# Optimization experiments

Hardware: AMD Instinct MI355X
Metric: run time of the kernel (lower is better)

Reference implementation:

```python
import jax, jax.numpy as jnp
import numpy as np

VISION_TOKEN_TYPE = 1
B, L, D, FF = 2, 2048, 1024, 4096


def setup_inputs() -> dict:
    key = jax.random.key(0)
    ks = jax.random.split(key, 8)
    s_in = 1.0 / np.sqrt(D)
    s_ff = 1.0 / np.sqrt(FF)
    return {
        "hidden_states": jax.random.normal(ks[0], (B, L, D), dtype=jnp.float32),
        "token_type_ids": jax.random.randint(ks[1], (B, L), 0, 2, dtype=jnp.int64),
        "v_gate": jax.random.normal(ks[2], (FF, D), dtype=jnp.float32) * s_in,
        "v_up": jax.random.normal(ks[3], (FF, D), dtype=jnp.float32) * s_in,
        "v_down": jax.random.normal(ks[4], (D, FF), dtype=jnp.float32) * s_ff,
        "l_gate": jax.random.normal(ks[5], (FF, D), dtype=jnp.float32) * s_in,
        "l_up": jax.random.normal(ks[6], (FF, D), dtype=jnp.float32) * s_in,
        "l_down": jax.random.normal(ks[7], (D, FF), dtype=jnp.float32) * s_ff,
    }


def _swiglu_mlp(x, w_gate, w_up, w_down):
    # x: (B, L, D); torch Linear stores weight as (out, in) -> contract on last dim
    g = jax.nn.silu(jnp.einsum("bld,fd->blf", x, w_gate))
    u = jnp.einsum("bld,fd->blf", x, w_up)
    return jnp.einsum("blf,df->bld", g * u, w_down)


def _vision_mask(token_type_ids):
    # vision token iff this token AND the next token are vision type; last col False
    t = token_type_ids == VISION_TOKEN_TYPE
    inner = t[:, :-1] & t[:, 1:]
    return jnp.concatenate([inner, jnp.zeros((t.shape[0], 1), dtype=bool)], axis=1)


def reference(hidden_states, token_type_ids, v_gate, v_up, v_down, l_gate, l_up, l_down):
    vision_mask = _vision_mask(token_type_ids)  # (B, L) bool
    vis_out = _swiglu_mlp(hidden_states, v_gate, v_up, v_down)
    lang_out = _swiglu_mlp(hidden_states, l_gate, l_up, l_down)
    return jnp.where(vision_mask[:, :, None], vis_out, lang_out)
```

## Files before the change

### kernel.cpp

```cpp
#include <hip/hip_runtime.h>
#include <hip/hip_bf16.h>
#include <stdint.h>


#define TOKENS 4096
#define SEQ    2048
#define DIM    1024
#define FFDIM  4096
#define MAXPAD 4608

typedef __attribute__((ext_vector_type(8))) short bf16x8;
typedef __attribute__((ext_vector_type(4))) float f32x4;

#define GAS __attribute__((address_space(1)))
#define LAS __attribute__((address_space(3)))

__device__ inline unsigned short f2bf(float x) {
    union { float f; unsigned int u; } c; c.f = x;
    unsigned int r = c.u + 0x7FFFu + ((c.u >> 16) & 1u);
    return (unsigned short)(r >> 16);
}
__device__ inline float bf2f(unsigned short u) {
    union { unsigned int i; float f; } c; c.i = ((unsigned int)u) << 16;
    return c.f;
}

struct __align__(16) us8 { unsigned short v[8]; };

__global__ __launch_bounds__(1024) void scan_kernel(const int* __restrict__ tt,
                                                    int* __restrict__ src_of,
                                                    int* __restrict__ counts) {
    __shared__ int wsum[16];
    const int tid  = threadIdx.x;
    const int lane = tid & 63;
    const int wav  = tid >> 6;

    for (int i = tid; i < MAXPAD; i += 1024) src_of[i] = -1;

    const int t0 = tid * 4;
    int v[4], cnt = 0;
#pragma unroll
    for (int j = 0; j < 4; ++j) {
        const int t = t0 + j;
        const int l = t & (SEQ - 1);
        int vis = 0;
        if (l < SEQ - 1) vis = (tt[t] == 1) & (tt[t + 1] == 1);
        v[j] = vis; cnt += vis;
    }

    int s = cnt;
#pragma unroll
    for (int off = 1; off < 64; off <<= 1) {
        const int o = __shfl_up(s, off, 64);
        if (lane >= off) s += o;
    }
    if (lane == 63) wsum[wav] = s;
    __syncthreads();
    if (wav == 0 && lane < 16) {
        int w = wsum[lane];
#pragma unroll
        for (int off = 1; off < 16; off <<= 1) {
            const int o = __shfl_up(w, off, 16);
            if (lane >= off) w += o;
        }
        wsum[lane] = w;
    }
    __syncthreads();

    const int wbase  = wav ? wsum[wav - 1] : 0;
    const int incl   = wbase + s;
    const int excl   = incl - cnt;
    const int totalV = wsum[15];
    const int padNv  = (totalV + 127) & ~127;
    int pv = excl;
    int pl = padNv + (t0 - excl);
#pragma unroll
    for (int j = 0; j < 4; ++j) {
        const int t = t0 + j;
        if (v[j]) src_of[pv++] = t; else src_of[pl++] = t;
    }
    if (tid == 0) {
        const int Nl = TOKENS - totalV;
        counts[0] = padNv;
        counts[1] = padNv + ((Nl + 127) & ~127);
    }
}

__device__ inline void gather_body(const float* __restrict__ hs, const int* __restrict__ src_of,
                                   unsigned short* __restrict__ Xg, int gid) {
    const int row = gid >> 7;
    const int c   = (gid & 127) * 8;
    const int src = src_of[row];
    us8 o;
    if (src >= 0) {
        const float4 a = *reinterpret_cast<const float4*>(hs + (size_t)src * DIM + c);
        const float4 b = *reinterpret_cast<const float4*>(hs + (size_t)src * DIM + c + 4);
        o.v[0] = f2bf(a.x); o.v[1] = f2bf(a.y); o.v[2] = f2bf(a.z); o.v[3] = f2bf(a.w);
        o.v[4] = f2bf(b.x); o.v[5] = f2bf(b.y); o.v[6] = f2bf(b.z); o.v[7] = f2bf(b.w);
    } else {
#pragma unroll
        for (int j = 0; j < 8; ++j) o.v[j] = 0;
    }
    *reinterpret_cast<us8*>(Xg + (size_t)row * DIM + c) = o;
}

__global__ void gather_cast(const float* __restrict__ hs, const int* __restrict__ src_of,
                            unsigned short* __restrict__ Xg) {
    gather_body(hs, src_of, Xg, blockIdx.x * 256 + threadIdx.x);
}

__device__ inline void cast8(const float* __restrict__ in, unsigned short* __restrict__ out, int i) {
    const float4 a = *reinterpret_cast<const float4*>(in + i);
    const float4 b = *reinterpret_cast<const float4*>(in + i + 4);
    us8 o;
    o.v[0] = f2bf(a.x); o.v[1] = f2bf(a.y); o.v[2] = f2bf(a.z); o.v[3] = f2bf(a.w);
    o.v[4] = f2bf(b.x); o.v[5] = f2bf(b.y); o.v[6] = f2bf(b.z); o.v[7] = f2bf(b.w);
    *reinterpret_cast<us8*>(out + i) = o;
}

__global__ void prep_kernel(const float* __restrict__ hs, const int* __restrict__ src_of,
                            unsigned short* __restrict__ Xg,
                            const float* __restrict__ s0, const float* __restrict__ s1,
                            const float* __restrict__ s2, const float* __restrict__ s3,
                            const float* __restrict__ s4, const float* __restrict__ s5,
                            unsigned short* __restrict__ d0, unsigned short* __restrict__ d1,
                            unsigned short* __restrict__ d2, unsigned short* __restrict__ d3,
                            unsigned short* __restrict__ d4, unsigned short* __restrict__ d5) {
    const int m = blockIdx.y;
    if (m == 0) {
        gather_body(hs, src_of, Xg, blockIdx.x * 256 + threadIdx.x);
    } else {
        const int i = (blockIdx.x * 256 + threadIdx.x) * 8;
        if (i >= FFDIM * DIM) return;
        const float* s = (m == 1) ? s0 : (m == 2) ? s1 : (m == 3) ? s2 : (m == 4) ? s3 : (m == 5) ? s4 : s5;
        unsigned short* d = (m == 1) ? d0 : (m == 2) ? d1 : (m == 3) ? d2 : (m == 4) ? d3 : (m == 5) ? d4 : d5;
        cast8(s, d, i);
    }
}

__global__ void cast4_kernel(const float* __restrict__ s0, const float* __restrict__ s1,
                             const float* __restrict__ s2, const float* __restrict__ s3,
                             unsigned short* __restrict__ d0, unsigned short* __restrict__ d1,
                             unsigned short* __restrict__ d2, unsigned short* __restrict__ d3) {
    const int i = (blockIdx.x * 256 + threadIdx.x) * 8;
    const int m = blockIdx.y;
    const float* s = (m == 0) ? s0 : (m == 1) ? s1 : (m == 2) ? s2 : s3;
    unsigned short* d = (m == 0) ? d0 : (m == 1) ? d1 : (m == 2) ? d2 : d3;
    cast8(s, d, i);
}

__global__ void cast2_kernel(const float* __restrict__ s0, const float* __restrict__ s1,
                             unsigned short* __restrict__ d0, unsigned short* __restrict__ d1) {
    const int i = (blockIdx.x * 256 + threadIdx.x) * 8;
    const float* s = blockIdx.y ? s1 : s0;
    unsigned short* d = blockIdx.y ? d1 : d0;
    cast8(s, d, i);
}

__global__ __launch_bounds__(256, 2) void gemm_p1(
    const unsigned short* __restrict__ A,
    const unsigned short* __restrict__ B0_v, const unsigned short* __restrict__ B1_v,
    const unsigned short* __restrict__ B0_l, const unsigned short* __restrict__ B1_l,
    unsigned short* __restrict__ H,
    const int* __restrict__ counts)
{
    __shared__ unsigned short Ls[256 * 64];

    const int m0 = blockIdx.y * 128;
    const int padNv = counts[0], padTot = counts[1];
    if (m0 >= padTot) return;
    const int expert = (m0 >= padNv);
    const unsigned short* B0 = expert ? B0_l : B0_v;
    const unsigned short* B1 = expert ? B1_l : B1_v;

    const int tid  = threadIdx.x;
    const int wid  = tid >> 6;
    const int lane = tid & 63;
    const int n0   = blockIdx.x * 64;

    constexpr int NI = 8;
    const unsigned short* src[NI];
    int loff[NI];
    const int cs = ((lane & 7) ^ (lane >> 3)) * 8;
#pragma unroll
    for (int i = 0; i < NI; ++i) {
        const int g = wid * 64 + i * 8 + (lane >> 3);
        const unsigned short* p;
        if (g < 128) {
            p = A + (size_t)(m0 + g) * DIM;
        } else {
            const int br = g - 128;
            p = (br < 64) ? (B0 + (size_t)(n0 + br) * DIM) : (B1 + (size_t)(n0 + br - 64) * DIM);
        }
        src[i] = p + cs;
        loff[i] = (wid * 64 + i * 8) * 64;
    }

    const int rlo = lane & 15;
    const int sw7 = rlo & 7;

    f32x4 acc[2][8];
#pragma unroll
    for (int i = 0; i < 2; ++i)
#pragma unroll
        for (int j = 0; j < 8; ++j)
            acc[i][j] = (f32x4){0.f, 0.f, 0.f, 0.f};

    const int NKT = DIM / 64;
#pragma unroll 1
    for (int kt = 0; kt < NKT; ++kt) {
        if (kt) __syncthreads();
        const int c = kt * 64;
#pragma unroll
        for (int i = 0; i < NI; ++i)
            __builtin_amdgcn_global_load_lds((const GAS void*)(src[i] + c),
                                             (LAS void*)&Ls[loff[i]], 16, 0, 0);
        asm volatile("s_waitcnt vmcnt(0)" ::: "memory");
        __syncthreads();

#pragma unroll
        for (int kh = 0; kh < 2; ++kh) {
            const int kc    = (lane >> 4) + kh * 4;
            const int swoff = (kc ^ sw7) * 8;
            const bf16x8 af0 = *reinterpret_cast<const bf16x8*>(&Ls[(wid * 32 + rlo) * 64 + swoff]);
            const bf16x8 af1 = *reinterpret_cast<const bf16x8*>(&Ls[(wid * 32 + 16 + rlo) * 64 + swoff]);
#pragma unroll
            for (int n = 0; n < 8; ++n) {
                const bf16x8 bfr = *reinterpret_cast<const bf16x8*>(&Ls[(128 + n * 16 + rlo) * 64 + swoff]);
                acc[0][n] = __builtin_amdgcn_mfma_f32_16x16x32_bf16(af0, bfr, acc[0][n], 0, 0, 0);
                acc[1][n] = __builtin_amdgcn_mfma_f32_16x16x32_bf16(af1, bfr, acc[1][n], 0, 0, 0);
            }
        }
    }

    const int rbase = m0 + wid * 32 + ((lane >> 4) * 4);
    const int cin   = lane & 15;
#pragma unroll
    for (int fr = 0; fr < 2; ++fr)
#pragma unroll
        for (int reg = 0; reg < 4; ++reg) {
            const int row = rbase + fr * 16 + reg;
#pragma unroll
            for (int n = 0; n < 4; ++n) {
                const float g = acc[fr][n][reg];
                const float u = acc[fr][n + 4][reg];
                const float h = g / (1.0f + __expf(-g)) * u;
                H[(size_t)row * FFDIM + n0 + n * 16 + cin] = f2bf(h);
            }
        }
}

__global__ __launch_bounds__(256, 2) void gemm_p2(
    const unsigned short* __restrict__ A,
    const unsigned short* __restrict__ Bd_v, const unsigned short* __restrict__ Bd_l,
    unsigned short* __restrict__ P,
    const int* __restrict__ counts)
{
    __shared__ unsigned short Ls[2][256 * 64];

    const int m0 = blockIdx.y * 128;
    const int padNv = counts[0], padTot = counts[1];
    if (m0 >= padTot) return;
    const unsigned short* B0 = (m0 >= padNv) ? Bd_l : Bd_v;

    const int tid  = threadIdx.x;
    const int wid  = tid >> 6;
    const int lane = tid & 63;
    const int wr   = wid >> 1;
    const int wc   = wid & 1;
    const int n0   = blockIdx.x * 128;
    const int kbase = blockIdx.z * (FFDIM / 2);

    constexpr int NI = 8;
    const unsigned short* src[NI];
    int loff[NI];
    const int cs = ((lane & 7) ^ (lane >> 3)) * 8;
#pragma unroll
    for (int i = 0; i < NI; ++i) {
        const int g = wid * 64 + i * 8 + (lane >> 3);
        const unsigned short* p = (g < 128)
            ? A + (size_t)(m0 + g) * FFDIM
            : B0 + (size_t)(n0 + g - 128) * FFDIM;
        src[i] = p + kbase + cs;
        loff[i] = (wid * 64 + i * 8) * 64;
    }

#define STAGE2(buf, kkt) do { \
    const int _c = (kkt) * 64; \
    _Pragma("unroll") \
    for (int i = 0; i < NI; ++i) \
        __builtin_amdgcn_global_load_lds((const GAS void*)(src[i] + _c), \
                                         (LAS void*)&Ls[buf][loff[i]], 16, 0, 0); \
} while (0)

    const int rlo = lane & 15;
    const int sw7 = rlo & 7;

    f32x4 acc[4][4];
#pragma unroll
    for (int i = 0; i < 4; ++i)
#pragma unroll
        for (int j = 0; j < 4; ++j)
            acc[i][j] = (f32x4){0.f, 0.f, 0.f, 0.f};

    STAGE2(0, 0);

    const int NKT = (FFDIM / 2) / 64;
    bf16x8 af[4], bf[4];
#pragma unroll 1
    for (int kt = 0; kt < NKT; ++kt) {
        const int cur = kt & 1;

        asm volatile("" ::: "memory");
        __builtin_amdgcn_s_barrier();
        asm volatile("" ::: "memory");

        if (kt + 1 < NKT) {
            STAGE2(cur ^ 1, kt + 1);
            asm volatile("s_waitcnt vmcnt(8)" ::: "memory");
        } else {
            asm volatile("s_waitcnt vmcnt(0)" ::: "memory");
        }

        asm volatile("" ::: "memory");
        __builtin_amdgcn_s_barrier();
        asm volatile("" ::: "memory");

#pragma unroll
        for (int kh = 0; kh < 2; ++kh) {
            const int kc    = (lane >> 4) + kh * 4;
            const int swoff = (kc ^ sw7) * 8;
#pragma unroll
            for (int i = 0; i < 4; ++i)
                af[i] = *reinterpret_cast<const bf16x8*>(&Ls[cur][(wr * 64 + i * 16 + rlo) * 64 + swoff]);
#pragma unroll
            for (int j = 0; j < 4; ++j)
                bf[j] = *reinterpret_cast<const bf16x8*>(&Ls[cur][(128 + wc * 64 + j * 16 + rlo) * 64 + swoff]);

            __builtin_amdgcn_s_setprio(1);
#pragma unroll
            for (int i = 0; i < 4; ++i)
#pragma unroll
                for (int j = 0; j < 4; ++j)
                    acc[i][j] = __builtin_amdgcn_mfma_f32_16x16x32_bf16(af[i], bf[j], acc[i][j], 0, 0, 0);
            __builtin_amdgcn_s_setprio(0);
        }
    }
#undef STAGE2

    unsigned short* Pz = P + (size_t)blockIdx.z * MAXPAD * DIM;
    const int rbase = m0 + wr * 64 + ((lane >> 4) * 4);
    const int cin   = lane & 15;
#pragma unroll
    for (int i = 0; i < 4; ++i)
#pragma unroll
        for (int reg = 0; reg < 4; ++reg) {
            const int row = rbase + i * 16 + reg;
#pragma unroll
            for (int j = 0; j < 4; ++j)
                Pz[(size_t)row * DIM + n0 + wc * 64 + j * 16 + cin] = f2bf(acc[i][j][reg]);
        }
}

__global__ void reduce_kernel(const unsigned short* __restrict__ P,
                              const int* __restrict__ src_of,
                              float* __restrict__ O) {
    const int gid = blockIdx.x * 256 + threadIdx.x;
    const int row = gid >> 7;
    const int c   = (gid & 127) * 8;
    const int src = src_of[row];
    if (src < 0) return;
    const us8 a = *reinterpret_cast<const us8*>(P + (size_t)row * DIM + c);
    const us8 b = *reinterpret_cast<const us8*>(P + (size_t)(MAXPAD + row) * DIM + c);
    float4 o0, o1;
    o0.x = bf2f(a.v[0]) + bf2f(b.v[0]);
    o0.y = bf2f(a.v[1]) + bf2f(b.v[1]);
    o0.z = bf2f(a.v[2]) + bf2f(b.v[2]);
    o0.w = bf2f(a.v[3]) + bf2f(b.v[3]);
    o1.x = bf2f(a.v[4]) + bf2f(b.v[4]);
    o1.y = bf2f(a.v[5]) + bf2f(b.v[5]);
    o1.z = bf2f(a.v[6]) + bf2f(b.v[6]);
    o1.w = bf2f(a.v[7]) + bf2f(b.v[7]);
    float* dst = O + (size_t)src * DIM + c;
    *reinterpret_cast<float4*>(dst)     = o0;
    *reinterpret_cast<float4*>(dst + 4) = o1;
}

extern "C" void kernel_launch(void* const* d_in, const int* in_sizes, int n_in,
                              void* d_out, int out_size, void* d_ws, size_t ws_size,
                              hipStream_t stream) {
    const float* hs = (const float*)d_in[0];
    const int*   tt = (const int*)d_in[1];
    const float* w_vg = (const float*)d_in[2];
    const float* w_vu = (const float*)d_in[3];
    const float* w_vd = (const float*)d_in[4];
    const float* w_lg = (const float*)d_in[5];
    const float* w_lu = (const float*)d_in[6];
    const float* w_ld = (const float*)d_in[7];
    float* out = (float*)d_out;
    char* ws = (char*)d_ws;

    const size_t MATB = (size_t)FFDIM * DIM * 2;
    const size_t XGB  = (size_t)MAXPAD * DIM * 2;
    const size_t HSZ  = (size_t)MAXPAD * FFDIM * 2;

    int* counts = (int*)ws;
    int* src_of = (int*)(ws + 64);
    unsigned short* Xg = (unsigned short*)(ws + 32768);

    const int NELEM = FFDIM * DIM;
    const size_t need_big = 32768 + XGB + 6 * MATB + HSZ;

    scan_kernel<<<1, 1024, 0, stream>>>(tt, src_of, counts);

    if (ws_size >= need_big) {
        unsigned short* Wg_v = (unsigned short*)(ws + 32768 + XGB);
        unsigned short* Wu_v = (unsigned short*)(ws + 32768 + XGB + MATB);
        unsigned short* Wg_l = (unsigned short*)(ws + 32768 + XGB + MATB * 2);
        unsigned short* Wu_l = (unsigned short*)(ws + 32768 + XGB + MATB * 3);
        unsigned short* Wd_v = (unsigned short*)(ws + 32768 + XGB + MATB * 4);
        unsigned short* Wd_l = (unsigned short*)(ws + 32768 + XGB + MATB * 5);
        unsigned short* H    = (unsigned short*)(ws + 32768 + XGB + MATB * 6);
        unsigned short* Part = Wg_v;

        dim3 gp(MAXPAD * 128 / 256, 7);
        prep_kernel<<<gp, 256, 0, stream>>>(hs, src_of, Xg,
                                            w_vg, w_vu, w_lg, w_lu, w_vd, w_ld,
                                            Wg_v, Wu_v, Wg_l, Wu_l, Wd_v, Wd_l);

        dim3 g1(FFDIM / 64, MAXPAD / 128);
        gemm_p1<<<g1, 256, 0, stream>>>(Xg, Wg_v, Wu_v, Wg_l, Wu_l, H, counts);

        dim3 g2(DIM / 128, MAXPAD / 128, 2);
        gemm_p2<<<g2, 256, 0, stream>>>(H, Wd_v, Wd_l, Part, counts);

        reduce_kernel<<<MAXPAD * 128 / 256, 256, 0, stream>>>(Part, src_of, out);
    } else {
        unsigned short* Wg_v = (unsigned short*)(ws + 32768 + XGB);
        unsigned short* Wu_v = (unsigned short*)(ws + 32768 + XGB + MATB);
        unsigned short* Wg_l = (unsigned short*)(ws + 32768 + XGB + MATB * 2);
        unsigned short* Wu_l = (unsigned short*)(ws + 32768 + XGB + MATB * 3);
        unsigned short* H    = (unsigned short*)(ws + 32768 + XGB + MATB * 4);
        unsigned short* Wd_v = (unsigned short*)(ws + 32768);
        unsigned short* Wd_l = (unsigned short*)(ws + 32768 + MATB);
        unsigned short* Part = (unsigned short*)(ws + 32768 + MATB * 2);

        gather_cast<<<MAXPAD * 128 / 256, 256, 0, stream>>>(hs, src_of, Xg);

        dim3 gc4(NELEM / 2048, 4);
        cast4_kernel<<<gc4, 256, 0, stream>>>(w_vg, w_vu, w_lg, w_lu, Wg_v, Wu_v, Wg_l, Wu_l);

        dim3 g1(FFDIM / 64, MAXPAD / 128);
        gemm_p1<<<g1, 256, 0, stream>>>(Xg, Wg_v, Wu_v, Wg_l, Wu_l, H, counts);

        dim3 gc2(NELEM / 2048, 2);
        cast2_kernel<<<gc2, 256, 0, stream>>>(w_vd, w_ld, Wd_v, Wd_l);

        dim3 g2(DIM / 128, MAXPAD / 128, 2);
        gemm_p2<<<g2, 256, 0, stream>>>(H, Wd_v, Wd_l, Part, counts);

        reduce_kernel<<<MAXPAD * 128 / 256, 256, 0, stream>>>(Part, src_of, out);
    }
}
```

Measured before the change: 183.2 us.

## Enlarge gate/up GEMM tile to 256x128 with double-buffered LDS pipeline

Rewrites the first fused gate/up GEMM to use 512-thread blocks computing a 256-row by 128-column tile for both gate and up. LDS is double-buffered so the next K slice loads while the current one feeds MFMAs, using a four-phase interleaved schedule with explicit waitcnt, barriers and setprio. Expert token padding is raised from 128 to 256 rows so the larger M tiles never straddle the vision/language boundary. The aim is more operand reuse per byte loaded and hidden global latency. The cost is more padded rows, about 128KB of LDS per block which limits occupancy to one block per CU, and a fragile hand-written barrier and waitcnt sequence.

```diff
diff --git a/kernel.cpp b/kernel.cpp
--- a/kernel.cpp
+++ b/kernel.cpp
@@ -71,7 +71,7 @@
     const int incl   = wbase + s;
     const int excl   = incl - cnt;
     const int totalV = wsum[15];
-    const int padNv  = (totalV + 127) & ~127;
+    const int padNv  = (totalV + 255) & ~255;
     int pv = excl;
     int pl = padNv + (t0 - excl);
 #pragma unroll
@@ -82,7 +82,7 @@
     if (tid == 0) {
         const int Nl = TOKENS - totalV;
         counts[0] = padNv;
-        counts[1] = padNv + ((Nl + 127) & ~127);
+        counts[1] = padNv + ((Nl + 255) & ~255);
     }
 }
 
@@ -157,97 +157,197 @@
     cast8(s, d, i);
 }
 
-__global__ __launch_bounds__(256, 2) void gemm_p1(
+__global__ __launch_bounds__(512, 2) void gemm_p1(
     const unsigned short* __restrict__ A,
     const unsigned short* __restrict__ B0_v, const unsigned short* __restrict__ B1_v,
     const unsigned short* __restrict__ B0_l, const unsigned short* __restrict__ B1_l,
     unsigned short* __restrict__ H,
     const int* __restrict__ counts)
 {
-    __shared__ unsigned short Ls[256 * 64];
-
-    const int m0 = blockIdx.y * 128;
+    __shared__ unsigned short Ls[2][512 * 64];
+
+    const int m0 = blockIdx.y * 256;
     const int padNv = counts[0], padTot = counts[1];
     if (m0 >= padTot) return;
     const int expert = (m0 >= padNv);
-    const unsigned short* B0 = expert ? B0_l : B0_v;
-    const unsigned short* B1 = expert ? B1_l : B1_v;
+    const unsigned short* Wg = expert ? B0_l : B0_v;
+    const unsigned short* Wu = expert ? B1_l : B1_v;
 
     const int tid  = threadIdx.x;
     const int wid  = tid >> 6;
     const int lane = tid & 63;
-    const int n0   = blockIdx.x * 64;
-
-    constexpr int NI = 8;
-    const unsigned short* src[NI];
-    int loff[NI];
-    const int cs = ((lane & 7) ^ (lane >> 3)) * 8;
-#pragma unroll
-    for (int i = 0; i < NI; ++i) {
-        const int g = wid * 64 + i * 8 + (lane >> 3);
-        const unsigned short* p;
-        if (g < 128) {
-            p = A + (size_t)(m0 + g) * DIM;
-        } else {
-            const int br = g - 128;
-            p = (br < 64) ? (B0 + (size_t)(n0 + br) * DIM) : (B1 + (size_t)(n0 + br - 64) * DIM);
-        }
-        src[i] = p + cs;
-        loff[i] = (wid * 64 + i * 8) * 64;
-    }
+    const int wr   = wid >> 2;
+    const int wc   = wid & 3;
+    const int n0   = blockIdx.x * 128;
+
+    const int cs   = ((lane & 7) ^ (lane >> 3)) * 8;
+    const int rsub = wid * 8 + (lane >> 3);
+    const int dW   = wid * 8 * 64;
+
+    const unsigned short* pA0 = A  + (size_t)(m0 +   0 + rsub) * DIM + cs;
+    const unsigned short* pA1 = A  + (size_t)(m0 +  64 + rsub) * DIM + cs;
+    const unsigned short* pA2 = A  + (size_t)(m0 + 128 + rsub) * DIM + cs;
+    const unsigned short* pA3 = A  + (size_t)(m0 + 192 + rsub) * DIM + cs;
+    const unsigned short* pG0 = Wg + (size_t)(n0 +   0 + rsub) * DIM + cs;
+    const unsigned short* pG1 = Wg + (size_t)(n0 +  64 + rsub) * DIM + cs;
+    const unsigned short* pU0 = Wu + (size_t)(n0 +   0 + rsub) * DIM + cs;
+    const unsigned short* pU1 = Wu + (size_t)(n0 +  64 + rsub) * DIM + cs;
+
+    unsigned short* L0 = &Ls[0][0];
+    unsigned short* L1 = &Ls[1][0];
+
+#define GLD(p, Ld, dst, ko) __builtin_amdgcn_global_load_lds( \
+        (const GAS void*)((p) + (ko)), (LAS void*)&(Ld)[(dst) + dW], 16, 0, 0)
+#define STA0(Ld, ko) do { GLD(pA0, Ld,   0 * 64, ko); GLD(pA1, Ld,  64 * 64, ko); } while (0)
+#define STA1(Ld, ko) do { GLD(pA2, Ld, 128 * 64, ko); GLD(pA3, Ld, 192 * 64, ko); } while (0)
+#define STB0(Ld, ko) do { GLD(pG0, Ld, 256 * 64, ko); GLD(pG1, Ld, 320 * 64, ko); } while (0)
+#define STB1(Ld, ko) do { GLD(pU0, Ld, 384 * 64, ko); GLD(pU1, Ld, 448 * 64, ko); } while (0)
+#define BAR() do { asm volatile("" ::: "memory"); \
+        __builtin_amdgcn_s_barrier(); asm volatile("" ::: "memory"); } while (0)
 
     const int rlo = lane & 15;
     const int sw7 = rlo & 7;
-
-    f32x4 acc[2][8];
-#pragma unroll
-    for (int i = 0; i < 2; ++i)
-#pragma unroll
-        for (int j = 0; j < 8; ++j)
-            acc[i][j] = (f32x4){0.f, 0.f, 0.f, 0.f};
+    bf16x8 af[4][2], bB[2][2];
+
+#define READA(Lc, QA) do { \
+    _Pragma("unroll") \
+    for (int kh = 0; kh < 2; ++kh) { \
+        const int swoff = (((lane >> 4) + kh * 4) ^ sw7) * 8; \
+        _Pragma("unroll") \
+        for (int i = 0; i < 4; ++i) \
+            af[i][kh] = *reinterpret_cast<const bf16x8*>( \
+                &(Lc)[((QA) * 128 + wr * 64 + i * 16 + rlo) * 64 + swoff]); \
+    } } while (0)
+#define READB(Lc, QB) do { \
+    _Pragma("unroll") \
+    for (int kh = 0; kh < 2; ++kh) { \
+        const int swoff = (((lane >> 4) + kh * 4) ^ sw7) * 8; \
+        _Pragma("unroll") \
+        for (int j = 0; j < 2; ++j) \
+            bB[j][kh] = *reinterpret_cast<const bf16x8*>( \
+                &(Lc)[(256 + (QB) * 128 + wc * 32 + j * 16 + rlo) * 64 + swoff]); \
+    } } while (0)
+#define MFMAQ(QA, ACC) do { \
+    __builtin_amdgcn_s_setprio(1); \
+    _Pragma("unroll") \
+    for (int kh = 0; kh < 2; ++kh) \
+        _Pragma("unroll") \
+        for (int i = 0; i < 4; ++i) \
+            _Pragma("unroll") \
+            for (int j = 0; j < 2; ++j) \
+                ACC[QA][i][j] = __builtin_amdgcn_mfma_f32_16x16x32_bf16( \
+                    af[i][kh], bB[j][kh], ACC[QA][i][j], 0, 0, 0); \
+    __builtin_amdgcn_s_setprio(0); } while (0)
+
+    f32x4 accg[2][4][2], accu[2][4][2];
+#pragma unroll
+    for (int qa = 0; qa < 2; ++qa)
+#pragma unroll
+        for (int i = 0; i < 4; ++i)
+#pragma unroll
+            for (int j = 0; j < 2; ++j) {
+                accg[qa][i][j] = (f32x4){0.f, 0.f, 0.f, 0.f};
+                accu[qa][i][j] = (f32x4){0.f, 0.f, 0.f, 0.f};
+            }
+
+    STA0(L0, 0); STB0(L0, 0); STA1(L0, 0); STB1(L0, 0);
+    asm volatile("s_waitcnt vmcnt(0)" ::: "memory");
+    BAR();
 
     const int NKT = DIM / 64;
+
 #pragma unroll 1
-    for (int kt = 0; kt < NKT; ++kt) {
-        if (kt) __syncthreads();
-        const int c = kt * 64;
-#pragma unroll
-        for (int i = 0; i < NI; ++i)
-            __builtin_amdgcn_global_load_lds((const GAS void*)(src[i] + c),
-                                             (LAS void*)&Ls[loff[i]], 16, 0, 0);
+    for (int t = 0; t < NKT - 1; ++t) {
+        unsigned short* Lc = (t & 1) ? L1 : L0;
+        unsigned short* Ln = (t & 1) ? L0 : L1;
+        const int ko = (t + 1) * 64;
+
+        READA(Lc, 0); READB(Lc, 0);
+        STA0(Ln, ko);
+        BAR();
+        asm volatile("s_waitcnt lgkmcnt(0)" ::: "memory");
+        MFMAQ(0, accg);
+        asm volatile("s_waitcnt vmcnt(4)" ::: "memory");
+        BAR();
+
+        READA(Lc, 1);
+        STB0(Ln, ko);
+        BAR();
+        asm volatile("s_waitcnt lgkmcnt(0)" ::: "memory");
+        MFMAQ(1, accg);
+        asm volatile("s_waitcnt vmcnt(4)" ::: "memory");
+        BAR();
+
+        READB(Lc, 1);
+        STA1(Ln, ko);
+        BAR();
+        asm volatile("s_waitcnt lgkmcnt(0)" ::: "memory");
+        MFMAQ(1, accu);
+        BAR();
+
+        READA(Lc, 0);
+        STB1(Ln, ko);
+        BAR();
+        asm volatile("s_waitcnt lgkmcnt(0)" ::: "memory");
+        MFMAQ(0, accu);
+        asm volatile("s_waitcnt vmcnt(4)" ::: "memory");
+        BAR();
+    }
+
+    {
+        unsigned short* Lc = L1;
+        READA(Lc, 0); READB(Lc, 0);
+        BAR();
+        asm volatile("s_waitcnt lgkmcnt(0)" ::: "memory");
+        MFMAQ(0, accg);
+        asm volatile("s_waitcnt vmcnt(2)" ::: "memory");
+        BAR();
+
+        READA(Lc, 1);
+        BAR();
+        asm volatile("s_waitcnt lgkmcnt(0)" ::: "memory");
+        MFMAQ(1, accg);
         asm volatile("s_waitcnt vmcnt(0)" ::: "memory");
-        __syncthreads();
-
-#pragma unroll
-        for (int kh = 0; kh < 2; ++kh) {
-            const int kc    = (lane >> 4) + kh * 4;
-            const int swoff = (kc ^ sw7) * 8;
-            const bf16x8 af0 = *reinterpret_cast<const bf16x8*>(&Ls[(wid * 32 + rlo) * 64 + swoff]);
-            const bf16x8 af1 = *reinterpret_cast<const bf16x8*>(&Ls[(wid * 32 + 16 + rlo) * 64 + swoff]);
-#pragma unroll
-            for (int n = 0; n < 8; ++n) {
-                const bf16x8 bfr = *reinterpret_cast<const bf16x8*>(&Ls[(128 + n * 16 + rlo) * 64 + swoff]);
-                acc[0][n] = __builtin_amdgcn_mfma_f32_16x16x32_bf16(af0, bfr, acc[0][n], 0, 0, 0);
-                acc[1][n] = __builtin_amdgcn_mfma_f32_16x16x32_bf16(af1, bfr, acc[1][n], 0, 0, 0);
+        BAR();
+
+        READB(Lc, 1);
+        BAR();
+        asm volatile("s_waitcnt lgkmcnt(0)" ::: "memory");
+        MFMAQ(1, accu);
+        BAR();
+
+        READA(Lc, 0);
+        BAR();
+        asm volatile("s_waitcnt lgkmcnt(0)" ::: "memory");
+        MFMAQ(0, accu);
+    }
+#undef READA
+#undef READB
+#undef MFMAQ
+#undef STA0
+#undef STA1
+#undef STB0
+#undef STB1
+#undef GLD
+#undef BAR
+
+    const int rb = m0 + wr * 64 + ((lane >> 4) * 4);
+    const int cb = n0 + wc * 32 + (lane & 15);
+#pragma unroll
+    for (int qa = 0; qa < 2; ++qa)
+#pragma unroll
+        for (int i = 0; i < 4; ++i)
+#pragma unroll
+            for (int reg = 0; reg < 4; ++reg) {
+                const int row = rb + qa * 128 + i * 16 + reg;
+#pragma unroll
+                for (int j = 0; j < 2; ++j) {
+                    const float g = accg[qa][i][j][reg];
+                    const float u = accu[qa][i][j][reg];
+                    const float hv = g / (1.0f + __expf(-g)) * u;
+                    H[(size_t)row * FFDIM + cb + j * 16] = f2bf(hv);
+                }
             }
-        }
-    }
-
-    const int rbase = m0 + wid * 32 + ((lane >> 4) * 4);
-    const int cin   = lane & 15;
-#pragma unroll
-    for (int fr = 0; fr < 2; ++fr)
-#pragma unroll
-        for (int reg = 0; reg < 4; ++reg) {
-            const int row = rbase + fr * 16 + reg;
-#pragma unroll
-            for (int n = 0; n < 4; ++n) {
-                const float g = acc[fr][n][reg];
-                const float u = acc[fr][n + 4][reg];
-                const float h = g / (1.0f + __expf(-g)) * u;
-                H[(size_t)row * FFDIM + n0 + n * 16 + cin] = f2bf(h);
-            }
-        }
 }
 
 __global__ __launch_bounds__(256, 2) void gemm_p2(
@@ -428,8 +528,8 @@
                                             w_vg, w_vu, w_lg, w_lu, w_vd, w_ld,
                                             Wg_v, Wu_v, Wg_l, Wu_l, Wd_v, Wd_l);
 
-        dim3 g1(FFDIM / 64, MAXPAD / 128);
-        gemm_p1<<<g1, 256, 0, stream>>>(Xg, Wg_v, Wu_v, Wg_l, Wu_l, H, counts);
+        dim3 g1(FFDIM / 128, MAXPAD / 256);
+        gemm_p1<<<g1, 512, 0, stream>>>(Xg, Wg_v, Wu_v, Wg_l, Wu_l, H, counts);
 
         dim3 g2(DIM / 128, MAXPAD / 128, 2);
         gemm_p2<<<g2, 256, 0, stream>>>(H, Wd_v, Wd_l, Part, counts);
@@ -450,8 +550,8 @@
         dim3 gc4(NELEM / 2048, 4);
         cast4_kernel<<<gc4, 256, 0, stream>>>(w_vg, w_vu, w_lg, w_lu, Wg_v, Wu_v, Wg_l, Wu_l);
 
-        dim3 g1(FFDIM / 64, MAXPAD / 128);
-        gemm_p1<<<g1, 256, 0, stream>>>(Xg, Wg_v, Wu_v, Wg_l, Wu_l, H, counts);
+        dim3 g1(FFDIM / 128, MAXPAD / 256);
+        gemm_p1<<<g1, 512, 0, stream>>>(Xg, Wg_v, Wu_v, Wg_l, Wu_l, H, counts);
 
         dim3 gc2(NELEM / 2048, 2);
         cast2_kernel<<<gc2, 256, 0, stream>>>(w_vd, w_ld, Wd_v, Wd_l);
```

New measurement: 197.3 us. 1.08x slower.

## Trade double-buffered LDS pipeline for higher occupancy in GEMM kernels

Applied to the files above, without the earlier changes.

Raises the launch_bounds occupancy hint from 2 to 4 blocks per CU for both GEMM kernels. In gemm_p2 it replaces the double-buffered LDS prefetch pipeline with a single buffer, a full vmcnt(0) wait and plain __syncthreads, and drops the s_setprio hints. The goal is to hide memory latency through more resident blocks rather than explicit prefetch. The cost is losing load/compute overlap within a block and possible register spills from the tighter register limit.

```diff
diff --git a/kernel.cpp b/kernel.cpp
--- a/kernel.cpp
+++ b/kernel.cpp
@@ -157,7 +157,7 @@
     cast8(s, d, i);
 }
 
-__global__ __launch_bounds__(256, 2) void gemm_p1(
+__global__ __launch_bounds__(256, 4) void gemm_p1(
     const unsigned short* __restrict__ A,
     const unsigned short* __restrict__ B0_v, const unsigned short* __restrict__ B1_v,
     const unsigned short* __restrict__ B0_l, const unsigned short* __restrict__ B1_l,
@@ -250,13 +250,13 @@
         }
 }
 
-__global__ __launch_bounds__(256, 2) void gemm_p2(
+__global__ __launch_bounds__(256, 4) void gemm_p2(
     const unsigned short* __restrict__ A,
     const unsigned short* __restrict__ Bd_v, const unsigned short* __restrict__ Bd_l,
     unsigned short* __restrict__ P,
     const int* __restrict__ counts)
 {
-    __shared__ unsigned short Ls[2][256 * 64];
+    __shared__ unsigned short Ls[256 * 64];
 
     const int m0 = blockIdx.y * 128;
     const int padNv = counts[0], padTot = counts[1];
@@ -285,14 +285,6 @@
         loff[i] = (wid * 64 + i * 8) * 64;
     }
 
-#define STAGE2(buf, kkt) do { \
-    const int _c = (kkt) * 64; \
-    _Pragma("unroll") \
-    for (int i = 0; i < NI; ++i) \
-        __builtin_amdgcn_global_load_lds((const GAS void*)(src[i] + _c), \
-                                         (LAS void*)&Ls[buf][loff[i]], 16, 0, 0); \
-} while (0)
-
     const int rlo = lane & 15;
     const int sw7 = rlo & 7;
 
@@ -302,29 +294,19 @@
 #pragma unroll
         for (int j = 0; j < 4; ++j)
             acc[i][j] = (f32x4){0.f, 0.f, 0.f, 0.f};
-
-    STAGE2(0, 0);
 
     const int NKT = (FFDIM / 2) / 64;
     bf16x8 af[4], bf[4];
 #pragma unroll 1
     for (int kt = 0; kt < NKT; ++kt) {
-        const int cur = kt & 1;
-
-        asm volatile("" ::: "memory");
-        __builtin_amdgcn_s_barrier();
-        asm volatile("" ::: "memory");
-
-        if (kt + 1 < NKT) {
-            STAGE2(cur ^ 1, kt + 1);
-            asm volatile("s_waitcnt vmcnt(8)" ::: "memory");
-        } else {
-            asm volatile("s_waitcnt vmcnt(0)" ::: "memory");
-        }
-
-        asm volatile("" ::: "memory");
-        __builtin_amdgcn_s_barrier();
-        asm volatile("" ::: "memory");
+        if (kt) __syncthreads();
+        const int c = kt * 64;
+#pragma unroll
+        for (int i = 0; i < NI; ++i)
+            __builtin_amdgcn_global_load_lds((const GAS void*)(src[i] + c),
+                                             (LAS void*)&Ls[loff[i]], 16, 0, 0);
+        asm volatile("s_waitcnt vmcnt(0)" ::: "memory");
+        __syncthreads();
 
 #pragma unroll
         for (int kh = 0; kh < 2; ++kh) {
@@ -332,21 +314,18 @@
             const int swoff = (kc ^ sw7) * 8;
 #pragma unroll
             for (int i = 0; i < 4; ++i)
-                af[i] = *reinterpret_cast<const bf16x8*>(&Ls[cur][(wr * 64 + i * 16 + rlo) * 64 + swoff]);
+                af[i] = *reinterpret_cast<const bf16x8*>(&Ls[(wr * 64 + i * 16 + rlo) * 64 + swoff]);
 #pragma unroll
             for (int j = 0; j < 4; ++j)
-                bf[j] = *reinterpret_cast<const bf16x8*>(&Ls[cur][(128 + wc * 64 + j * 16 + rlo) * 64 + swoff]);
-
-            __builtin_amdgcn_s_setprio(1);
+                bf[j] = *reinterpret_cast<const bf16x8*>(&Ls[(128 + wc * 64 + j * 16 + rlo) * 64 + swoff]);
+
 #pragma unroll
             for (int i = 0; i < 4; ++i)
 #pragma unroll
                 for (int j = 0; j < 4; ++j)
                     acc[i][j] = __builtin_amdgcn_mfma_f32_16x16x32_bf16(af[i], bf[j], acc[i][j], 0, 0, 0);
-            __builtin_amdgcn_s_setprio(0);
-        }
-    }
-#undef STAGE2
+        }
+    }
 
     unsigned short* Pz = P + (size_t)blockIdx.z * MAXPAD * DIM;
     const int rbase = m0 + wr * 64 + ((lane >> 4) * 4);
```

New measurement: 177.2 us (median of 2 runs). -3.3%, faster.
